# Kernel optimization log

Hardware: AMD Instinct MI355X
Metric: run time of the kernel (lower is better)

## Reference

```python
import jax, jax.numpy as jnp
import numpy as np

B, T, M = 8, 512, 80
U = 896          # RNN_Size (even)
C = 256          # Class


def setup_inputs() -> dict:
    key = jax.random.key(0)
    ks = jax.random.split(key, 13)
    s = 0.05
    d = {
        'mels': jax.random.normal(ks[0], (B, T, M), jnp.float32),
        'Wk':  jax.random.normal(ks[1], (M + 3, 3 * U), jnp.float32) * s,
        'Wr':  jax.random.normal(ks[2], (U, 3 * U), jnp.float32) * s,
        'b':   jax.random.normal(ks[3], (2, 3 * U), jnp.float32) * s,
        'W1c': jax.random.normal(ks[4], (U // 2, U // 2), jnp.float32) * s,
        'b1c': jax.random.normal(ks[5], (U // 2,), jnp.float32) * s,
        'W2c': jax.random.normal(ks[6], (U // 2, C), jnp.float32) * s,
        'b2c': jax.random.normal(ks[7], (C,), jnp.float32) * s,
        'W1f': jax.random.normal(ks[8], (U // 2, U // 2), jnp.float32) * s,
        'b1f': jax.random.normal(ks[9], (U // 2,), jnp.float32) * s,
        'W2f': jax.random.normal(ks[10], (U // 2, C), jnp.float32) * s,
        'b2f': jax.random.normal(ks[11], (C,), jnp.float32) * s,
    }
    return d


def reference(mels, Wk, Wr, b, W1c, b1c, W2c, b2c, W1f, b1f, W2f, b2f):
    # Keras GRUCell (reset_after=True) step.
    def gru(x, h):
        mx = x @ Wk + b[0]                     # [B, 3U]
        mi = h @ Wr + b[1]                     # [B, 3U]
        xz, xr, xh = jnp.split(mx, 3, axis=-1)
        iz, ir, ih = jnp.split(mi, 3, axis=-1)
        z = jax.nn.sigmoid(xz + iz)
        r = jax.nn.sigmoid(xr + ir)
        hh = jnp.tanh(xh + r * ih)
        return z * h + (1.0 - z) * hh

    def head(h, W1, b1, W2, b2):
        return jax.nn.relu(h @ W1 + b1) @ W2 + b2

    Bv = mels.shape[0]
    Tv = mels.shape[1]
    keys = jax.random.split(jax.random.key(42), Tv)
    mels_t = jnp.swapaxes(mels, 0, 1)          # [T, B, M]

    def step(carry, xs):
        coarse, fine, hidden = carry           # [B,1],[B,1],[B,U]
        mel, key = xs
        kc, kf = jax.random.split(key)
        dummy = jnp.zeros_like(coarse)
        # coarse pass (hidden NOT updated, faithful to original)
        x0 = jnp.concatenate([mel, coarse, fine, dummy], axis=-1)
        h0 = gru(x0, hidden)
        logit_c = head(h0[:, :U // 2], W1c, b1c, W2c, b2c)
        # original feeds softmax probs into tf.random.categorical (which
        # expects logits) -- reproduce that faithfully.
        probs_c = jax.nn.softmax(logit_c, axis=-1)
        new_c = jax.random.categorical(kc, probs_c, axis=-1).astype(mels.dtype)[:, None]
        new_c_val = new_c / 255.0 * 2.0 - 1.0
        # fine pass (hidden IS updated)
        x1 = jnp.concatenate([mel, coarse, fine, new_c_val], axis=-1)
        h1 = gru(x1, hidden)
        logit_f = head(h1[:, U // 2:], W1f, b1f, W2f, b2f)
        probs_f = jax.nn.softmax(logit_f, axis=-1)
        new_f = jax.random.categorical(kf, probs_f, axis=-1).astype(mels.dtype)[:, None]
        new_f_val = new_f / 255.0 * 2.0 - 1.0
        sample = (new_c * C + new_f) / 32767.5 - 1.0   # [B,1]
        return (new_c_val, new_f_val, h1), sample[:, 0]

    init = (jnp.zeros((Bv, 1), mels.dtype),
            jnp.zeros((Bv, 1), mels.dtype),
            jnp.zeros((Bv, U), mels.dtype))
    _, samples = jax.lax.scan(step, init, (mels_t, keys))
    return jnp.swapaxes(samples, 0, 1)         # [B, T]
```

## Files before the change

### kernel.cpp

```cpp
#include <hip/hip_runtime.h>
#include <cstdint>
#include <math.h>

#define U 896
#define HU 448
#define TU 2688
#define BB 8
#define TT 512
#define MM 80
#define CC 256
#define NTH 512
#define NBLK 188

__device__ __forceinline__ uint32_t rotl32(uint32_t v, int r){ return (v<<r)|(v>>(32-r)); }

__device__ void threefry(uint32_t k0, uint32_t k1, uint32_t x0, uint32_t x1,
                         uint32_t* o0, uint32_t* o1){
  uint32_t k2 = k0 ^ k1 ^ 0x1BD11BDAu;
  x0 += k0; x1 += k1;
  x0+=x1; x1=rotl32(x1,13); x1^=x0;
  x0+=x1; x1=rotl32(x1,15); x1^=x0;
  x0+=x1; x1=rotl32(x1,26); x1^=x0;
  x0+=x1; x1=rotl32(x1, 6); x1^=x0;
  x0+=k1; x1+=k2+1u;
  x0+=x1; x1=rotl32(x1,17); x1^=x0;
  x0+=x1; x1=rotl32(x1,29); x1^=x0;
  x0+=x1; x1=rotl32(x1,16); x1^=x0;
  x0+=x1; x1=rotl32(x1,24); x1^=x0;
  x0+=k2; x1+=k0+2u;
  x0+=x1; x1=rotl32(x1,13); x1^=x0;
  x0+=x1; x1=rotl32(x1,15); x1^=x0;
  x0+=x1; x1=rotl32(x1,26); x1^=x0;
  x0+=x1; x1=rotl32(x1, 6); x1^=x0;
  x0+=k0; x1+=k1+3u;
  x0+=x1; x1=rotl32(x1,17); x1^=x0;
  x0+=x1; x1=rotl32(x1,29); x1^=x0;
  x0+=x1; x1=rotl32(x1,16); x1^=x0;
  x0+=x1; x1=rotl32(x1,24); x1^=x0;
  x0+=k1; x1+=k2+4u;
  x0+=x1; x1=rotl32(x1,13); x1^=x0;
  x0+=x1; x1=rotl32(x1,15); x1^=x0;
  x0+=x1; x1=rotl32(x1,26); x1^=x0;
  x0+=x1; x1=rotl32(x1, 6); x1^=x0;
  x0+=k2; x1+=k0+5u;
  *o0 = x0; *o1 = x1;
}

__device__ float gumbel_from(uint32_t ka, uint32_t kb, uint32_t e){
  uint32_t o0, o1;
  threefry(ka, kb, 0u, e, &o0, &o1);
  uint32_t bits = o0 ^ o1;
  uint32_t m = bits >> 9;
  float u = (m == 0u) ? 1.17549435e-38f
                      : (__uint_as_float(m | 0x3f800000u) - 1.0f);
  float l1 = (float)log((double)u);
  float l2 = (float)log((double)(-l1));
  return -l2;
}

__device__ __forceinline__ float sig_f(float x){
  return (float)(0.5 + 0.5*tanh(0.5*(double)x));
}
__device__ __forceinline__ float tanh_f(float x){ return (float)tanh((double)x); }

__device__ __forceinline__ float gldf(const float* p){
  return __hip_atomic_load(p, __ATOMIC_RELAXED, __HIP_MEMORY_SCOPE_AGENT);
}
__device__ __forceinline__ void gstf(float* p, float v){
  __hip_atomic_store(p, v, __ATOMIC_RELAXED, __HIP_MEMORY_SCOPE_AGENT);
}
__device__ __forceinline__ int gldi(const int* p){
  return __hip_atomic_load(p, __ATOMIC_RELAXED, __HIP_MEMORY_SCOPE_AGENT);
}
__device__ __forceinline__ void gsti(int* p, int v){
  __hip_atomic_store(p, v, __ATOMIC_RELAXED, __HIP_MEMORY_SCOPE_AGENT);
}

__device__ __forceinline__ void wait_slots(const uint32_t* slots, int n, uint32_t tgt, int tid){
  if (tid < n){
    const uint32_t* p = slots + (size_t)tid*32;
    int it = 0;
    while (__hip_atomic_load(p, __ATOMIC_RELAXED, __HIP_MEMORY_SCOPE_AGENT) < tgt){
      __builtin_amdgcn_s_sleep(1);
      if (++it > (1<<22)) break;
    }
  }
  __syncthreads();
}
__device__ __forceinline__ void publish_slot(uint32_t* slot, uint32_t v, int tid){
  __syncthreads();
  if (tid == 0)
    __hip_atomic_store(slot, v, __ATOMIC_RELEASE, __HIP_MEMORY_SCOPE_AGENT);
}

__device__ __forceinline__ void fma4(float4& a, const float4& w, float h){
  a.x += w.x*h; a.y += w.y*h; a.z += w.z*h; a.w += w.w*h;
}

__device__ __forceinline__ void bf8(float4* a){
  #pragma unroll
  for (int d=8; d<64; d<<=1){
    #pragma unroll
    for (int b=0;b<8;++b){
      a[b].x += __shfl_xor(a[b].x, d);
      a[b].y += __shfl_xor(a[b].y, d);
      a[b].z += __shfl_xor(a[b].z, d);
      a[b].w += __shfl_xor(a[b].w, d);
    }
  }
}

__global__ __launch_bounds__(256) void k_keys(uint32_t* __restrict__ kc, uint32_t* __restrict__ kf){
  int t = blockIdx.x*256 + threadIdx.x;
  if (t >= TT) return;
  uint32_t ka, kb;
  threefry(0u, 42u, 0u, (uint32_t)t, &ka, &kb);
  uint32_t c0,c1,f0,f1;
  threefry(ka, kb, 0u, 0u, &c0, &c1);
  threefry(ka, kb, 0u, 1u, &f0, &f1);
  kc[2*t] = c0; kc[2*t+1] = c1;
  kf[2*t] = f0; kf[2*t+1] = f1;
}

#define O_SH1   0
#define O_SH1HI 1024
#define O_SFV   2048
#define O_SG    3072
#define O_SY1C  6656
#define O_SLC   13824
#define O_SY1F  15872
#define O_SLF   23040
#define O_KC    25088
#define O_KF    29184
#define O_NCV   33280
#define O_FVS   33344
#define O_NCI   33408
#define O_PRE   33536
#define O_IHB   119552
#define O_HGL   148224
#define O_H0C   205568
#define O_Y1C   219904
#define O_Y1F   234240
#define O_LGTC  248576
#define O_LGTF  256768
#define WS_ZERO 264960

__global__ __launch_bounds__(NTH, 2) void wavernn_persist(
    const float* __restrict__ mels, const float* __restrict__ Wk,
    const float* __restrict__ Wr,  const float* __restrict__ bias,
    const float* __restrict__ W1c, const float* __restrict__ b1c,
    const float* __restrict__ W2c, const float* __restrict__ b2c,
    const float* __restrict__ W1f, const float* __restrict__ b1f,
    const float* __restrict__ W2f, const float* __restrict__ b2f,
    float* __restrict__ out, char* __restrict__ ws)
{
  uint32_t* SH1   = (uint32_t*)(ws + O_SH1);
  uint32_t* SH1HI = (uint32_t*)(ws + O_SH1HI);
  uint32_t* SFV   = (uint32_t*)(ws + O_SFV);
  uint32_t* SG    = (uint32_t*)(ws + O_SG);
  uint32_t* SY1C  = (uint32_t*)(ws + O_SY1C);
  uint32_t* SLC   = (uint32_t*)(ws + O_SLC);
  uint32_t* SY1F  = (uint32_t*)(ws + O_SY1F);
  uint32_t* SLF   = (uint32_t*)(ws + O_SLF);
  const uint32_t* kc = (const uint32_t*)(ws + O_KC);
  const uint32_t* kf = (const uint32_t*)(ws + O_KF);
  float* ncvB = (float*)(ws + O_NCV);
  float* fvsB = (float*)(ws + O_FVS);
  int*   nci  = (int*)  (ws + O_NCI);
  float* pre  = (float*)(ws + O_PRE);
  float* ihb  = (float*)(ws + O_IHB);
  float* hgl  = (float*)(ws + O_HGL);
  float* h0c  = (float*)(ws + O_H0C);
  float* y1c  = (float*)(ws + O_Y1C);
  float* y1f  = (float*)(ws + O_Y1F);
  float* lgtC = (float*)(ws + O_LGTC);
  float* lgtF = (float*)(ws + O_LGTF);

  __shared__ __align__(16) char smem[46080];
  const int bk = blockIdx.x, tid = threadIdx.x;

  if (bk < 28){
    const int c4i = tid & 7, ks = tid >> 3;
    const int k0 = ks*14;
    const int lane = tid & 63, wv = tid >> 6;
    const int U0 = bk*32;
    const int cb0 = U0 + c4i*4;
    float* hlf   = (float*)smem;
    float* wredf = (float*)(smem + 32768);
    float* gbuf  = (float*)(smem + 41984);
    const int xk = 896 + ks*2;
    const int r0 = ((xk   < 978) ? xk   : 978) - 896;
    const int r1 = ((xk+1 < 978) ? xk+1 : 978) - 896;

    for (int t=0; t<TT; ++t){
      wait_slots(SH1, 8, (uint32_t)t, tid);
      const int hs = (t&1)*7168;
      for (int i=tid;i<8192;i+=NTH){
        const int b = i>>10, k = i&1023;
        float v;
        if (k < 896)      v = gldf(hgl + hs + b*896 + k);
        else if (k < 976) v = mels[((size_t)b*TT + t)*MM + (k-896)];
        else if (k == 976)v = gldf(ncvB + ((t+1)&1)*8 + b);
        else              v = 0.f;
        hlf[i] = v;
      }
      __syncthreads();

      for (int g=0; g<3; ++g){
        const int cbg = g*896 + cb0;
        float4 aW[8], aX[8];
        #pragma unroll
        for (int b=0;b<8;++b){ aW[b]=make_float4(0,0,0,0); aX[b]=make_float4(0,0,0,0); }
        #pragma unroll 2
        for (int j=0;j<14;++j){
          const float4 w = *(const float4*)(Wr + (size_t)(k0+j)*TU + cbg);
          #pragma unroll
          for (int b=0;b<8;++b) fma4(aW[b], w, hlf[b*1024 + k0 + j]);
        }
        {
          const float4 w0 = *(const float4*)(Wk + (size_t)r0*TU + cbg);
          const float4 w1 = *(const float4*)(Wk + (size_t)r1*TU + cbg);
          #pragma unroll
          for (int b=0;b<8;++b){
            fma4(aX[b], w0, hlf[b*1024 + 896 + ks*2]);
            fma4(aX[b], w1, hlf[b*1024 + 897 + ks*2]);
          }
        }
        if (g < 2){
          #pragma unroll
          for (int b=0;b<8;++b){
            aW[b].x += aX[b].x; aW[b].y += aX[b].y;
            aW[b].z += aX[b].z; aW[b].w += aX[b].w;
          }
          bf8(aW);
          if (lane < 8){
            float* dst = wredf + wv*288 + lane*36;
            #pragma unroll
            for (int b=0;b<8;++b) *(float4*)(dst + b*4) = aW[b];
          }
          __syncthreads();
          if (tid < 256){
            const int b = tid>>5, ci = tid&31;
            float s = 0.f;
            #pragma unroll
            for (int w=0; w<8; ++w) s += wredf[w*288 + (ci>>2)*36 + b*4 + (ci&3)];
            const int col = g*896 + U0 + ci;
            const float val = s + bias[col] + bias[TU + col];
            gstf(pre + b*TU + col, val);
            gbuf[(b*32 + ci)*4 + g] = val;
          }
          __syncthreads();
        } else {
          bf8(aW);
          if (lane < 8){
            float* dst = wredf + wv*288 + lane*36;
            #pragma unroll
            for (int b=0;b<8;++b) *(float4*)(dst + b*4) = aW[b];
          }
          __syncthreads();
          if (tid < 256){
            const int b = tid>>5, ci = tid&31;
            float s = 0.f;
            #pragma unroll
            for (int w=0; w<8; ++w) s += wredf[w*288 + (ci>>2)*36 + b*4 + (ci&3)];
            const int u = U0 + ci;
            const float val = s + bias[TU + 1792 + u];
            gstf(ihb + b*896 + u, val);
            gbuf[(b*32 + ci)*4 + 3] = val;
          }
          __syncthreads();
          bf8(aX);
          if (lane < 8){
            float* dst = wredf + wv*288 + lane*36;
            #pragma unroll
            for (int b=0;b<8;++b) *(float4*)(dst + b*4) = aX[b];
          }
          __syncthreads();
          if (tid < 256){
            const int b = tid>>5, ci = tid&31;
            float s = 0.f;
            #pragma unroll
            for (int w=0; w<8; ++w) s += wredf[w*288 + (ci>>2)*36 + b*4 + (ci&3)];
            const int u = U0 + ci;
            const float val = s + bias[1792 + u];
            gstf(pre + b*TU + 1792 + u, val);
            gbuf[(b*32 + ci)*4 + 2] = val;
          }
          __syncthreads();
        }
      }

      if (bk < 14){
        wait_slots(SFV, 8, (uint32_t)t, tid);
        if (tid < 256){
          const int b = tid>>5, ub = tid&31, u = U0 + ub;
          const float fv = gldf(fvsB + ((t+1)&1)*8 + b);
          const float* gb = gbuf + (b*32 + ub)*4;
          const float az = gb[0] + fv*Wk[(size_t)81*TU + u];
          const float ar = gb[1] + fv*Wk[(size_t)81*TU + 896 + u];
          const float ax = gb[2] + fv*Wk[(size_t)81*TU + 1792 + u];
          const float z = sig_f(az), r = sig_f(ar);
          const float hh = tanh_f(ax + r*gb[3]);
          gstf(h0c + b*HU + u, z*hlf[b*1024 + u] + (1.0f - z)*hh);
        }
      }
      publish_slot(SG + bk*32, (uint32_t)(t+1), tid);
    }
  } else if (bk < 84){
    const int j = bk - 28;
    float* h0s = (float*)smem;
    float (*red2)[8] = (float(*)[8])(smem + 16384);
    const int c2 = tid&1, b1 = (tid>>1)&7, ks1 = tid>>4;
    const int colb = j*8 + c2*4, i0 = ks1*14;
    for (int t=0; t<TT; ++t){
      wait_slots(SG, 14, (uint32_t)(t+1), tid);
      for (int i=tid;i<3584;i+=NTH) h0s[i] = gldf(h0c + i);
      __syncthreads();
      float4 a = make_float4(0,0,0,0);
      #pragma unroll
      for (int i=0;i<14;++i){
        const float4 w = *(const float4*)(W1c + (size_t)(i0+i)*HU + colb);
        fma4(a, w, h0s[b1*HU + i0+i]);
      }
      *(float4*)&red2[tid][0] = a;
      __syncthreads();
      if (tid < 64){
        const int ci = tid&7, b = tid>>3;
        float s = 0.f;
        #pragma unroll
        for (int q=0;q<32;++q) s += red2[q*16 + b*2 + (ci>>2)][ci&3];
        const int col = j*8 + ci;
        gstf(y1c + b*HU + col, fmaxf(s + b1c[col], 0.0f));
      }
      publish_slot(SY1C + j*32, (uint32_t)(t+1), tid);
    }
  } else if (bk < 100){
    const int j = bk - 84;
    float* shs = (float*)smem;
    float (*red3)[8] = (float(*)[8])(smem + 16384);
    const int c4b = tid&3, b1 = (tid>>2)&7, ks1 = tid>>5;
    const int colb = j*16 + c4b*4, i0 = ks1*28;
    for (int t=0; t<TT; ++t){
      wait_slots(SY1C, 56, (uint32_t)(t+1), tid);
      for (int i=tid;i<3584;i+=NTH) shs[i] = gldf(y1c + i);
      __syncthreads();
      float4 a = make_float4(0,0,0,0);
      #pragma unroll
      for (int i=0;i<28;++i){
        const float4 w = *(const float4*)(W2c + (size_t)(i0+i)*CC + colb);
        fma4(a, w, shs[b1*HU + i0+i]);
      }
      *(float4*)&red3[tid][0] = a;
      __syncthreads();
      if (tid < 128){
        const int ci = tid&15, b = tid>>4;
        float s = 0.f;
        #pragma unroll
        for (int q=0;q<16;++q) s += red3[q*32 + b*4 + (ci>>2)][ci&3];
        const int col = j*16 + ci;
        gstf(lgtC + b*CC + col, s + b2c[col]);
      }
      publish_slot(SLC + j*32, (uint32_t)(t+1), tid);
    }
  } else if (bk < 108){
    const int b = bk - 100;
    float* sredf = (float*)smem;
    int*   sredi = (int*)(smem + 64);
    for (int t=0; t<TT; ++t){
      const float gmb = (tid<256) ? gumbel_from(kc[2*t], kc[2*t+1], (uint32_t)(b*CC + tid)) : 0.f;
      wait_slots(SLC, 16, (uint32_t)(t+1), tid);
      wait_slots(SG, 28, (uint32_t)(t+1), tid);
      const float logit = (tid<256) ? gldf(lgtC + b*CC + tid) : -3.402823466e38f;
      float m = logit;
      #pragma unroll
      for (int d=1; d<64; d<<=1) m = fmaxf(m, __shfl_xor(m, d));
      if ((tid&63)==0) sredf[tid>>6] = m;
      __syncthreads();
      const float mx = fmaxf(fmaxf(sredf[0],sredf[1]), fmaxf(sredf[2],sredf[3]));
      __syncthreads();
      const float e = (tid<256) ? (float)exp((double)(logit - mx)) : 0.f;
      float ss = e;
      #pragma unroll
      for (int d=1; d<64; d<<=1) ss += __shfl_xor(ss, d);
      if ((tid&63)==0) sredf[tid>>6] = ss;
      __syncthreads();
      const float sum = (sredf[0]+sredf[1])+(sredf[2]+sredf[3]);
      __syncthreads();
      float v = (tid<256) ? (e/sum + gmb) : -3.402823466e38f;
      int bi = (tid<256) ? tid : (1<<30);
      #pragma unroll
      for (int d=1; d<64; d<<=1){
        const float ov = __shfl_xor(v, d);
        const int   oi = __shfl_xor(bi, d);
        if (ov > v || (ov == v && oi < bi)){ v = ov; bi = oi; }
      }
      if ((tid&63)==0){ sredf[tid>>6] = v; sredi[tid>>6] = bi; }
      __syncthreads();
      float bv = sredf[0]; int nc = sredi[0];
      #pragma unroll
      for (int w=1; w<4; ++w){
        if (sredf[w] > bv || (sredf[w] == bv && sredi[w] < nc)){ bv = sredf[w]; nc = sredi[w]; }
      }
      if (tid==0){
        gsti(nci + b, nc);
        gstf(ncvB + (t&1)*8 + b, (float)nc/255.0f*2.0f - 1.0f);
      }
      const float ncv = (float)nc/255.0f*2.0f - 1.0f;
      const float fv = gldf(fvsB + ((t+1)&1)*8 + b);
      const int hsO = (t&1)*7168, hsN = ((t+1)&1)*7168;
      if (tid < 448){
        const int u = 448 + tid;
        const float az = gldf(pre + b*TU + u)        + fv*Wk[(size_t)81*TU + u]        + ncv*Wk[(size_t)82*TU + u];
        const float ar = gldf(pre + b*TU + 896 + u)  + fv*Wk[(size_t)81*TU + 896 + u]  + ncv*Wk[(size_t)82*TU + 896 + u];
        const float ax = gldf(pre + b*TU + 1792 + u) + fv*Wk[(size_t)81*TU + 1792 + u] + ncv*Wk[(size_t)82*TU + 1792 + u];
        const float ih = gldf(ihb + b*896 + u);
        const float z = sig_f(az), r = sig_f(ar);
        const float hh = tanh_f(ax + r*ih);
        gstf(hgl + hsN + b*896 + u, z*gldf(hgl + hsO + b*896 + u) + (1.0f - z)*hh);
      }
      publish_slot(SH1HI + b*32, (uint32_t)(t+1), tid);
      if (tid < 448){
        const int u = tid;
        const float az = gldf(pre + b*TU + u)        + fv*Wk[(size_t)81*TU + u]        + ncv*Wk[(size_t)82*TU + u];
        const float ar = gldf(pre + b*TU + 896 + u)  + fv*Wk[(size_t)81*TU + 896 + u]  + ncv*Wk[(size_t)82*TU + 896 + u];
        const float ax = gldf(pre + b*TU + 1792 + u) + fv*Wk[(size_t)81*TU + 1792 + u] + ncv*Wk[(size_t)82*TU + 1792 + u];
        const float ih = gldf(ihb + b*896 + u);
        const float z = sig_f(az), r = sig_f(ar);
        const float hh = tanh_f(ax + r*ih);
        gstf(hgl + hsN + b*896 + u, z*gldf(hgl + hsO + b*896 + u) + (1.0f - z)*hh);
      }
      publish_slot(SH1 + b*32, (uint32_t)(t+1), tid);
    }
  } else if (bk < 164){
    const int j = bk - 108;
    float* hfs = (float*)smem;
    float (*red2)[8] = (float(*)[8])(smem + 16384);
    const int c2 = tid&1, b1 = (tid>>1)&7, ks1 = tid>>4;
    const int colb = j*8 + c2*4, i0 = ks1*14;
    for (int t=0; t<TT; ++t){
      wait_slots(SH1HI, 8, (uint32_t)(t+1), tid);
      const int hsN = ((t+1)&1)*7168;
      for (int i=tid;i<3584;i+=NTH){
        const int b = i/HU, ii = i - b*HU;
        hfs[i] = gldf(hgl + hsN + b*U + HU + ii);
      }
      __syncthreads();
      float4 a = make_float4(0,0,0,0);
      #pragma unroll
      for (int i=0;i<14;++i){
        const float4 w = *(const float4*)(W1f + (size_t)(i0+i)*HU + colb);
        fma4(a, w, hfs[b1*HU + i0+i]);
      }
      *(float4*)&red2[tid][0] = a;
      __syncthreads();
      if (tid < 64){
        const int ci = tid&7, b = tid>>3;
        float s = 0.f;
        #pragma unroll
        for (int q=0;q<32;++q) s += red2[q*16 + b*2 + (ci>>2)][ci&3];
        const int col = j*8 + ci;
        gstf(y1f + b*HU + col, fmaxf(s + b1f[col], 0.0f));
      }
      publish_slot(SY1F + j*32, (uint32_t)(t+1), tid);
    }
  } else if (bk < 180){
    const int j = bk - 164;
    float* shs = (float*)smem;
    float (*red3)[8] = (float(*)[8])(smem + 16384);
    const int c4b = tid&3, b1 = (tid>>2)&7, ks1 = tid>>5;
    const int colb = j*16 + c4b*4, i0 = ks1*28;
    for (int t=0; t<TT; ++t){
      wait_slots(SY1F, 56, (uint32_t)(t+1), tid);
      for (int i=tid;i<3584;i+=NTH) shs[i] = gldf(y1f + i);
      __syncthreads();
      float4 a = make_float4(0,0,0,0);
      #pragma unroll
      for (int i=0;i<28;++i){
        const float4 w = *(const float4*)(W2f + (size_t)(i0+i)*CC + colb);
        fma4(a, w, shs[b1*HU + i0+i]);
      }
      *(float4*)&red3[tid][0] = a;
      __syncthreads();
      if (tid < 128){
        const int ci = tid&15, b = tid>>4;
        float s = 0.f;
        #pragma unroll
        for (int q=0;q<16;++q) s += red3[q*32 + b*4 + (ci>>2)][ci&3];
        const int col = j*16 + ci;
        gstf(lgtF + b*CC + col, s + b2f[col]);
      }
      publish_slot(SLF + j*32, (uint32_t)(t+1), tid);
    }
  } else {
    const int b = bk - 180;
    float* sredf = (float*)smem;
    int*   sredi = (int*)(smem + 64);
    for (int t=0; t<TT; ++t){
      const float gmb = (tid<256) ? gumbel_from(kf[2*t], kf[2*t+1], (uint32_t)(b*CC + tid)) : 0.f;
      wait_slots(SLF, 16, (uint32_t)(t+1), tid);
      const float logit = (tid<256) ? gldf(lgtF + b*CC + tid) : -3.402823466e38f;
      float m = logit;
      #pragma unroll
      for (int d=1; d<64; d<<=1) m = fmaxf(m, __shfl_xor(m, d));
      if ((tid&63)==0) sredf[tid>>6] = m;
      __syncthreads();
      const float mx = fmaxf(fmaxf(sredf[0],sredf[1]), fmaxf(sredf[2],sredf[3]));
      __syncthreads();
      const float e = (tid<256) ? (float)exp((double)(logit - mx)) : 0.f;
      float ss = e;
      #pragma unroll
      for (int d=1; d<64; d<<=1) ss += __shfl_xor(ss, d);
      if ((tid&63)==0) sredf[tid>>6] = ss;
      __syncthreads();
      const float sum = (sredf[0]+sredf[1])+(sredf[2]+sredf[3]);
      __syncthreads();
      float v = (tid<256) ? (e/sum + gmb) : -3.402823466e38f;
      int bi = (tid<256) ? tid : (1<<30);
      #pragma unroll
      for (int d=1; d<64; d<<=1){
        const float ov = __shfl_xor(v, d);
        const int   oi = __shfl_xor(bi, d);
        if (ov > v || (ov == v && oi < bi)){ v = ov; bi = oi; }
      }
      if ((tid&63)==0){ sredf[tid>>6] = v; sredi[tid>>6] = bi; }
      __syncthreads();
      float bv = sredf[0]; int nf = sredi[0];
      #pragma unroll
      for (int w=1; w<4; ++w){
        if (sredf[w] > bv || (sredf[w] == bv && sredi[w] < nf)){ bv = sredf[w]; nf = sredi[w]; }
      }
      if (tid==0){
        gstf(fvsB + (t&1)*8 + b, (float)nf/255.0f*2.0f - 1.0f);
        const int nc = gldi(nci + b);
        out[(size_t)b*TT + t] = ((float)nc*256.0f + (float)nf)/32767.5f - 1.0f;
      }
      publish_slot(SFV + b*32, (uint32_t)(t+1), tid);
    }
  }
}

extern "C" void kernel_launch(void* const* d_in, const int* in_sizes, int n_in,
                              void* d_out, int out_size, void* d_ws, size_t ws_size,
                              hipStream_t stream) {
  const float* mels = (const float*)d_in[0];
  const float* Wk   = (const float*)d_in[1];
  const float* Wr   = (const float*)d_in[2];
  const float* bias = (const float*)d_in[3];
  const float* W1c  = (const float*)d_in[4];
  const float* b1c  = (const float*)d_in[5];
  const float* W2c  = (const float*)d_in[6];
  const float* b2c  = (const float*)d_in[7];
  const float* W1f  = (const float*)d_in[8];
  const float* b1f  = (const float*)d_in[9];
  const float* W2f  = (const float*)d_in[10];
  const float* b2f  = (const float*)d_in[11];
  float* out = (float*)d_out;
  char* wsb = (char*)d_ws;

  uint32_t* kc = (uint32_t*)(wsb + O_KC);
  uint32_t* kf = (uint32_t*)(wsb + O_KF);

  hipMemsetAsync(d_ws, 0, WS_ZERO, stream);
  k_keys<<<2,256,0,stream>>>(kc, kf);

  void* args[] = { (void*)&mels, (void*)&Wk, (void*)&Wr, (void*)&bias,
                   (void*)&W1c, (void*)&b1c, (void*)&W2c, (void*)&b2c,
                   (void*)&W1f, (void*)&b1f, (void*)&W2f, (void*)&b2f,
                   (void*)&out, (void*)&wsb };
  hipLaunchCooperativeKernel((const void*)wavernn_persist, dim3(NBLK), dim3(NTH),
                             args, 0, stream);
}
```

Baseline: 20.09 ms.

## Fuse head layers into shared blocks with partial-logit reduction, drop spin sleep

Merges the separate W1 and W2 head stages for both coarse and fine passes into 28 blocks. Each block computes a 16-column slice of the ReLU hidden layer and multiplies it by the matching rows of W2, producing partial logits. The sampling blocks then sum the 28 partials, which removes one grid-wide synchronization hop per head per step. This cuts the persistent grid from 188 to 72 blocks. It also removes s_sleep from the spin-wait, lowering wake-up latency at the cost of more polling traffic and extra partial-logit memory.

```diff
diff --git a/kernel.cpp b/kernel.cpp
--- a/kernel.cpp
+++ b/kernel.cpp
@@ -10,7 +10,7 @@
 #define MM 80
 #define CC 256
 #define NTH 512
-#define NBLK 188
+#define NBLK 72
 
 __device__ __forceinline__ uint32_t rotl32(uint32_t v, int r){ return (v<<r)|(v>>(32-r)); }
 
@@ -81,8 +81,7 @@
     const uint32_t* p = slots + (size_t)tid*32;
     int it = 0;
     while (__hip_atomic_load(p, __ATOMIC_RELAXED, __HIP_MEMORY_SCOPE_AGENT) < tgt){
-      __builtin_amdgcn_s_sleep(1);
-      if (++it > (1<<22)) break;
+      if (++it > (1<<24)) break;
     }
   }
   __syncthreads();
@@ -126,24 +125,20 @@
 #define O_SH1HI 1024
 #define O_SFV   2048
 #define O_SG    3072
-#define O_SY1C  6656
-#define O_SLC   13824
-#define O_SY1F  15872
-#define O_SLF   23040
-#define O_KC    25088
-#define O_KF    29184
-#define O_NCV   33280
-#define O_FVS   33344
-#define O_NCI   33408
-#define O_PRE   33536
-#define O_IHB   119552
-#define O_HGL   148224
-#define O_H0C   205568
-#define O_Y1C   219904
-#define O_Y1F   234240
-#define O_LGTC  248576
-#define O_LGTF  256768
-#define WS_ZERO 264960
+#define O_SYC   6656
+#define O_SYF   10240
+#define O_KC    13824
+#define O_KF    17920
+#define O_NCV   22016
+#define O_FVS   22080
+#define O_NCI   22144
+#define O_PRE   22272
+#define O_IHB   108288
+#define O_HGL   136960
+#define O_H0C   194304
+#define O_PLC   208640
+#define O_PLF   438016
+#define WS_ZERO 667392
 
 __global__ __launch_bounds__(NTH, 2) void wavernn_persist(
     const float* __restrict__ mels, const float* __restrict__ Wk,
@@ -158,10 +153,8 @@
   uint32_t* SH1HI = (uint32_t*)(ws + O_SH1HI);
   uint32_t* SFV   = (uint32_t*)(ws + O_SFV);
   uint32_t* SG    = (uint32_t*)(ws + O_SG);
-  uint32_t* SY1C  = (uint32_t*)(ws + O_SY1C);
-  uint32_t* SLC   = (uint32_t*)(ws + O_SLC);
-  uint32_t* SY1F  = (uint32_t*)(ws + O_SY1F);
-  uint32_t* SLF   = (uint32_t*)(ws + O_SLF);
+  uint32_t* SYC   = (uint32_t*)(ws + O_SYC);
+  uint32_t* SYF   = (uint32_t*)(ws + O_SYF);
   const uint32_t* kc = (const uint32_t*)(ws + O_KC);
   const uint32_t* kf = (const uint32_t*)(ws + O_KF);
   float* ncvB = (float*)(ws + O_NCV);
@@ -171,10 +164,8 @@
   float* ihb  = (float*)(ws + O_IHB);
   float* hgl  = (float*)(ws + O_HGL);
   float* h0c  = (float*)(ws + O_H0C);
-  float* y1c  = (float*)(ws + O_Y1C);
-  float* y1f  = (float*)(ws + O_Y1F);
-  float* lgtC = (float*)(ws + O_LGTC);
-  float* lgtF = (float*)(ws + O_LGTF);
+  float* plgtC= (float*)(ws + O_PLC);
+  float* plgtF= (float*)(ws + O_PLF);
 
   __shared__ __align__(16) char smem[46080];
   const int bk = blockIdx.x, tid = threadIdx.x;
@@ -306,71 +297,91 @@
       }
       publish_slot(SG + bk*32, (uint32_t)(t+1), tid);
     }
-  } else if (bk < 84){
+  } else if (bk < 56){
     const int j = bk - 28;
-    float* h0s = (float*)smem;
-    float (*red2)[8] = (float(*)[8])(smem + 16384);
-    const int c2 = tid&1, b1 = (tid>>1)&7, ks1 = tid>>4;
-    const int colb = j*8 + c2*4, i0 = ks1*14;
+    float* hstg = (float*)smem;
+    float* red1 = (float*)(smem + 14336);
+    float* y1s  = (float*)(smem + 16384);
+    const int outp = tid & 127, ks4 = tid >> 7;
+    const int ob = outp >> 4, oc = outp & 15;
+    const int i0 = ks4*112;
+
     for (int t=0; t<TT; ++t){
       wait_slots(SG, 14, (uint32_t)(t+1), tid);
-      for (int i=tid;i<3584;i+=NTH) h0s[i] = gldf(h0c + i);
-      __syncthreads();
-      float4 a = make_float4(0,0,0,0);
-      #pragma unroll
-      for (int i=0;i<14;++i){
-        const float4 w = *(const float4*)(W1c + (size_t)(i0+i)*HU + colb);
-        fma4(a, w, h0s[b1*HU + i0+i]);
-      }
-      *(float4*)&red2[tid][0] = a;
-      __syncthreads();
-      if (tid < 64){
-        const int ci = tid&7, b = tid>>3;
+      for (int i=tid;i<3584;i+=NTH) hstg[i] = gldf(h0c + i);
+      __syncthreads();
+      {
         float s = 0.f;
+        const float* hb = hstg + ob*HU;
+        const float* wb = W1c + (size_t)i0*HU + j*16 + oc;
+        #pragma unroll 4
+        for (int i=0;i<112;++i) s += hb[i0+i]*wb[(size_t)i*HU];
+        red1[outp*4 + ks4] = s;
+      }
+      __syncthreads();
+      if (tid < 128){
+        const float v = (red1[tid*4+0]+red1[tid*4+1])+(red1[tid*4+2]+red1[tid*4+3]);
+        y1s[tid] = fmaxf(v + b1c[j*16 + (tid&15)], 0.0f);
+      }
+      __syncthreads();
+      #pragma unroll
+      for (int p=0;p<4;++p){
+        const int o2 = p*512 + tid;
+        const int b = o2 >> 8, cc = o2 & 255;
+        float s2 = 0.f;
         #pragma unroll
-        for (int q=0;q<32;++q) s += red2[q*16 + b*2 + (ci>>2)][ci&3];
-        const int col = j*8 + ci;
-        gstf(y1c + b*HU + col, fmaxf(s + b1c[col], 0.0f));
-      }
-      publish_slot(SY1C + j*32, (uint32_t)(t+1), tid);
+        for (int i=0;i<16;++i) s2 += y1s[b*16+i]*W2c[(size_t)(j*16+i)*CC + cc];
+        gstf(plgtC + j*2048 + o2, s2);
+      }
+      publish_slot(SYC + j*32, (uint32_t)(t+1), tid);
+
+      wait_slots(SH1HI, 8, (uint32_t)(t+1), tid);
+      const int hsN = ((t+1)&1)*7168;
+      for (int i=tid;i<3584;i+=NTH){
+        const int b = i/HU, ii = i - b*HU;
+        hstg[i] = gldf(hgl + hsN + b*U + HU + ii);
+      }
+      __syncthreads();
+      {
+        float s = 0.f;
+        const float* hb = hstg + ob*HU;
+        const float* wb = W1f + (size_t)i0*HU + j*16 + oc;
+        #pragma unroll 4
+        for (int i=0;i<112;++i) s += hb[i0+i]*wb[(size_t)i*HU];
+        red1[outp*4 + ks4] = s;
+      }
+      __syncthreads();
+      if (tid < 128){
+        const float v = (red1[tid*4+0]+red1[tid*4+1])+(red1[tid*4+2]+red1[tid*4+3]);
+        y1s[tid] = fmaxf(v + b1f[j*16 + (tid&15)], 0.0f);
+      }
+      __syncthreads();
+      #pragma unroll
+      for (int p=0;p<4;++p){
+        const int o2 = p*512 + tid;
+        const int b = o2 >> 8, cc = o2 & 255;
+        float s2 = 0.f;
+        #pragma unroll
+        for (int i=0;i<16;++i) s2 += y1s[b*16+i]*W2f[(size_t)(j*16+i)*CC + cc];
+        gstf(plgtF + j*2048 + o2, s2);
+      }
+      publish_slot(SYF + j*32, (uint32_t)(t+1), tid);
     }
-  } else if (bk < 100){
-    const int j = bk - 84;
-    float* shs = (float*)smem;
-    float (*red3)[8] = (float(*)[8])(smem + 16384);
-    const int c4b = tid&3, b1 = (tid>>2)&7, ks1 = tid>>5;
-    const int colb = j*16 + c4b*4, i0 = ks1*28;
-    for (int t=0; t<TT; ++t){
-      wait_slots(SY1C, 56, (uint32_t)(t+1), tid);
-      for (int i=tid;i<3584;i+=NTH) shs[i] = gldf(y1c + i);
-      __syncthreads();
-      float4 a = make_float4(0,0,0,0);
-      #pragma unroll
-      for (int i=0;i<28;++i){
-        const float4 w = *(const float4*)(W2c + (size_t)(i0+i)*CC + colb);
-        fma4(a, w, shs[b1*HU + i0+i]);
-      }
-      *(float4*)&red3[tid][0] = a;
-      __syncthreads();
-      if (tid < 128){
-        const int ci = tid&15, b = tid>>4;
-        float s = 0.f;
-        #pragma unroll
-        for (int q=0;q<16;++q) s += red3[q*32 + b*4 + (ci>>2)][ci&3];
-        const int col = j*16 + ci;
-        gstf(lgtC + b*CC + col, s + b2c[col]);
-      }
-      publish_slot(SLC + j*32, (uint32_t)(t+1), tid);
-    }
-  } else if (bk < 108){
-    const int b = bk - 100;
+  } else if (bk < 64){
+    const int b = bk - 56;
     float* sredf = (float*)smem;
     int*   sredi = (int*)(smem + 64);
     for (int t=0; t<TT; ++t){
       const float gmb = (tid<256) ? gumbel_from(kc[2*t], kc[2*t+1], (uint32_t)(b*CC + tid)) : 0.f;
-      wait_slots(SLC, 16, (uint32_t)(t+1), tid);
+      wait_slots(SYC, 28, (uint32_t)(t+1), tid);
       wait_slots(SG, 28, (uint32_t)(t+1), tid);
-      const float logit = (tid<256) ? gldf(lgtC + b*CC + tid) : -3.402823466e38f;
+      float logit = -3.402823466e38f;
+      if (tid < 256){
+        float s = 0.f;
+        #pragma unroll
+        for (int j=0;j<28;++j) s += gldf(plgtC + j*2048 + b*CC + tid);
+        logit = s + b2c[tid];
+      }
       float m = logit;
       #pragma unroll
       for (int d=1; d<64; d<<=1) m = fmaxf(m, __shfl_xor(m, d));
@@ -431,74 +442,20 @@
       }
       publish_slot(SH1 + b*32, (uint32_t)(t+1), tid);
     }
-  } else if (bk < 164){
-    const int j = bk - 108;
-    float* hfs = (float*)smem;
-    float (*red2)[8] = (float(*)[8])(smem + 16384);
-    const int c2 = tid&1, b1 = (tid>>1)&7, ks1 = tid>>4;
-    const int colb = j*8 + c2*4, i0 = ks1*14;
-    for (int t=0; t<TT; ++t){
-      wait_slots(SH1HI, 8, (uint32_t)(t+1), tid);
-      const int hsN = ((t+1)&1)*7168;
-      for (int i=tid;i<3584;i+=NTH){
-        const int b = i/HU, ii = i - b*HU;
-        hfs[i] = gldf(hgl + hsN + b*U + HU + ii);
-      }
-      __syncthreads();
-      float4 a = make_float4(0,0,0,0);
-      #pragma unroll
-      for (int i=0;i<14;++i){
-        const float4 w = *(const float4*)(W1f + (size_t)(i0+i)*HU + colb);
-        fma4(a, w, hfs[b1*HU + i0+i]);
-      }
-      *(float4*)&red2[tid][0] = a;
-      __syncthreads();
-      if (tid < 64){
-        const int ci = tid&7, b = tid>>3;
-        float s = 0.f;
-        #pragma unroll
-        for (int q=0;q<32;++q) s += red2[q*16 + b*2 + (ci>>2)][ci&3];
-        const int col = j*8 + ci;
-        gstf(y1f + b*HU + col, fmaxf(s + b1f[col], 0.0f));
-      }
-      publish_slot(SY1F + j*32, (uint32_t)(t+1), tid);
-    }
-  } else if (bk < 180){
-    const int j = bk - 164;
-    float* shs = (float*)smem;
-    float (*red3)[8] = (float(*)[8])(smem + 16384);
-    const int c4b = tid&3, b1 = (tid>>2)&7, ks1 = tid>>5;
-    const int colb = j*16 + c4b*4, i0 = ks1*28;
-    for (int t=0; t<TT; ++t){
-      wait_slots(SY1F, 56, (uint32_t)(t+1), tid);
-      for (int i=tid;i<3584;i+=NTH) shs[i] = gldf(y1f + i);
-      __syncthreads();
-      float4 a = make_float4(0,0,0,0);
-      #pragma unroll
-      for (int i=0;i<28;++i){
-        const float4 w = *(const float4*)(W2f + (size_t)(i0+i)*CC + colb);
-        fma4(a, w, shs[b1*HU + i0+i]);
-      }
-      *(float4*)&red3[tid][0] = a;
-      __syncthreads();
-      if (tid < 128){
-        const int ci = tid&15, b = tid>>4;
-        float s = 0.f;
-        #pragma unroll
-        for (int q=0;q<16;++q) s += red3[q*32 + b*4 + (ci>>2)][ci&3];
-        const int col = j*16 + ci;
-        gstf(lgtF + b*CC + col, s + b2f[col]);
-      }
-      publish_slot(SLF + j*32, (uint32_t)(t+1), tid);
-    }
   } else {
-    const int b = bk - 180;
+    const int b = bk - 64;
     float* sredf = (float*)smem;
     int*   sredi = (int*)(smem + 64);
     for (int t=0; t<TT; ++t){
       const float gmb = (tid<256) ? gumbel_from(kf[2*t], kf[2*t+1], (uint32_t)(b*CC + tid)) : 0.f;
-      wait_slots(SLF, 16, (uint32_t)(t+1), tid);
-      const float logit = (tid<256) ? gldf(lgtF + b*CC + tid) : -3.402823466e38f;
+      wait_slots(SYF, 28, (uint32_t)(t+1), tid);
+      float logit = -3.402823466e38f;
+      if (tid < 256){
+        float s = 0.f;
+        #pragma unroll
+        for (int j=0;j<28;++j) s += gldf(plgtF + j*2048 + b*CC + tid);
+        logit = s + b2f[tid];
+      }
       float m = logit;
       #pragma unroll
       for (int d=1; d<64; d<<=1) m = fmaxf(m, __shfl_xor(m, d));
```

After: 20.12 ms. No clear change (+0.2%).
